# Performance work log

Hardware: AMD Instinct MI355X
Metric: run time of the kernel (lower is better)

The kernel has to match this reference:

```python
import jax, jax.numpy as jnp
import numpy as np

B, L, N = 8, 5, 4096
RADIUS, K = 0.7, 32
SPATIAL_STRIDE = 16
TK, TSTRIDE = 3, 2  # temporal kernel / stride; temporal_padding=[1,1] replicate
DIM, DEPTH, HEADS, DIM_HEAD, MLP_DIM, OUT_DIM = 512, 5, 8, 64, 1024, 1088
INNER = HEADS * DIM_HEAD
N_ANCH = 64
NTOT = N + N_ANCH
M = NTOT // SPATIAL_STRIDE  # spatial anchors per output frame


def setup_inputs() -> dict:
    key = jax.random.key(0)
    ks = list(jax.random.split(key, 16))
    s = 0.02
    p = {}
    p["points"] = jax.random.uniform(ks[0], (B, L, N, 3), jnp.float32, -1.0, 1.0)
    p["conv_d_w"] = jax.random.normal(ks[1], (DIM, 4), jnp.float32) * s
    p["conv_f_w"] = jax.random.normal(ks[2], (DIM, 3), jnp.float32) * s
    p["pos_w"] = jax.random.normal(ks[3], (DIM, 4), jnp.float32) * s
    p["pos_b"] = jnp.zeros((DIM,), jnp.float32)
    p["ln1_g"] = jnp.ones((DEPTH, DIM)); p["ln1_b"] = jnp.zeros((DEPTH, DIM))
    p["qkv_w"] = jax.random.normal(ks[4], (DEPTH, DIM, 3 * INNER), jnp.float32) * s
    p["attn_out_w"] = jax.random.normal(ks[5], (DEPTH, INNER, DIM), jnp.float32) * s
    p["attn_out_b"] = jnp.zeros((DEPTH, DIM))
    p["ln2_g"] = jnp.ones((DEPTH, DIM)); p["ln2_b"] = jnp.zeros((DEPTH, DIM))
    p["ff1_w"] = jax.random.normal(ks[6], (DEPTH, DIM, MLP_DIM), jnp.float32) * s
    p["ff1_b"] = jnp.zeros((DEPTH, MLP_DIM))
    p["ff2_w"] = jax.random.normal(ks[7], (DEPTH, MLP_DIM, DIM), jnp.float32) * s
    p["ff2_b"] = jnp.zeros((DEPTH, DIM))
    p["head_ln_g"] = jnp.ones((DIM,)); p["head_ln_b"] = jnp.zeros((DIM,))
    p["head1_w"] = jax.random.normal(ks[8], (DIM, MLP_DIM), jnp.float32) * s
    p["head1_b"] = jnp.zeros((MLP_DIM,))
    p["head2_w"] = jax.random.normal(ks[9], (MLP_DIM, OUT_DIM), jnp.float32) * s
    p["head2_b"] = jnp.zeros((OUT_DIM,))
    return p


def _layer_norm(x, g, b, eps=1e-5):
    mu = jnp.mean(x, -1, keepdims=True)
    var = jnp.mean((x - mu) ** 2, -1, keepdims=True)
    return (x - mu) * jax.lax.rsqrt(var + eps) * g + b


def _anchor_grid():
    lin = jnp.linspace(-1.5, 1.5, 4)
    gx, gy, gz = jnp.meshgrid(lin, lin, lin, indexing="ij")
    return jnp.stack([gx.ravel(), gy.ravel(), gz.ravel()], -1)  # (64,3)


def _fps(pts, m):
    # furthest point sampling, pts (N,3) -> (m,) int32, first pick is index 0 (pointnet2 semantics)
    def step(carry, _):
        dist, last = carry
        d = jnp.sum((pts - pts[last]) ** 2, -1)
        dist = jnp.minimum(dist, d)
        return (dist, jnp.argmax(dist).astype(jnp.int32)), last
    init = (jnp.full((pts.shape[0],), 1e10, pts.dtype), jnp.int32(0))
    _, idx = jax.lax.scan(step, init, None, length=m)
    return idx


def _ball_query(anchors, pts, radius, k):
    # first k point indices within radius of each anchor; pad with first hit (0 if none)
    d2 = jnp.sum((anchors[:, None, :] - pts[None, :, :]) ** 2, -1)  # (M,N)
    n = pts.shape[0]
    cand = jnp.where(d2 < radius * radius, jnp.arange(n, dtype=jnp.int32), n)
    neg_topk, _ = jax.lax.top_k(-cand, k)  # k smallest indices, ascending
    idx = -neg_topk
    first = idx[:, :1]
    idx = jnp.where(idx == n, first, idx)
    return jnp.where(idx == n, 0, idx)


def _forward(points, conv_d_w, conv_f_w, pos_w, pos_b, ln1_g, ln1_b, qkv_w,
             attn_out_w, attn_out_b, ln2_g, ln2_b, ff1_w, ff1_b, ff2_w, ff2_b,
             head_ln_g, head_ln_b, head1_w, head1_b, head2_w, head2_b):
    anch = _anchor_grid()  # (64,3)
    pts = jnp.concatenate(
        [points[..., :3], jnp.broadcast_to(anch, (B, L, N_ANCH, 3))], axis=2)  # (B,L,NTOT,3)
    # replicate temporal padding [1,1]
    frames = jnp.concatenate([pts[:, :1], pts, pts[:, -1:]], axis=1)  # (B,L+2,NTOT,3)

    trad = (TK - 1) // 2
    nT = L + 2
    gather = jax.vmap(lambda p, i: p[i])
    out_xyz, out_feat = [], []
    for t in range(trad, nT - trad, TSTRIDE):
        f_t = frames[:, t]                                   # (B,NTOT,3)
        a_idx = jax.vmap(lambda p: _fps(p, M))(f_t)          # (B,M)
        a_xyz = gather(f_t, a_idx)                           # (B,M,3)
        feats_w = []
        for i in range(t - trad, t + trad + 1):
            nb = frames[:, i]                                # (B,NTOT,3)
            idx = jax.vmap(lambda a, p: _ball_query(a, p, RADIUS, K))(a_xyz, nb)  # (B,M,K)
            grouped = gather(nb, idx)                        # (B,M,K,3)
            disp = grouped - a_xyz[:, :, None, :]
            tdisp = jnp.full((B, M, K, 1), float(i - t), disp.dtype)
            disp4 = jnp.concatenate([disp, tdisp], -1)       # (B,M,K,4)
            # conv_f(features) + conv_d(displacement); features fed in are the xyz themselves
            feat = (jnp.einsum("bmkc,dc->bmkd", grouped, conv_f_w)
                    + jnp.einsum("bmkc,dc->bmkd", disp4, conv_d_w))
            feats_w.append(jnp.max(feat, axis=2))            # spatial max -> (B,M,DIM)
        out_feat.append(jnp.max(jnp.stack(feats_w, 0), axis=0))  # temporal max
        out_xyz.append(a_xyz)

    nF = len(out_xyz)
    xyzs = jnp.stack(out_xyz, 1)                             # (B,nF,M,3)
    feats = jnp.stack(out_feat, 1).reshape(B, nF * M, DIM)
    tcol = jnp.broadcast_to(
        jnp.arange(1, nF + 1, dtype=xyzs.dtype)[None, :, None, None], (B, nF, M, 1))
    xyzts = jnp.concatenate([xyzs, tcol], -1).reshape(B, nF * M, 4)
    x = jnp.einsum("bnc,dc->bnd", xyzts, pos_w) + pos_b + feats  # (B,T,DIM); emb_relu=False

    scale = DIM_HEAD ** -0.5
    for l in range(DEPTH):
        xn = _layer_norm(x, ln1_g[l], ln1_b[l])
        q, k, v = jnp.split(xn @ qkv_w[l], 3, axis=-1)
        rs = lambda a: a.reshape(B, -1, HEADS, DIM_HEAD)
        q, k, v = rs(q), rs(k), rs(v)
        att = jax.nn.softmax(jnp.einsum("bqhd,bkhd->bhqk", q, k) * scale, axis=-1)
        o = jnp.einsum("bhqk,bkhd->bqhd", att, v).reshape(B, -1, INNER)
        x = x + o @ attn_out_w[l] + attn_out_b[l]
        xn = _layer_norm(x, ln2_g[l], ln2_b[l])
        x = x + jax.nn.gelu(xn @ ff1_w[l] + ff1_b[l], approximate=False) @ ff2_w[l] + ff2_b[l]

    x = jnp.max(x, axis=1)                                   # (B,DIM)
    x = _layer_norm(x, head_ln_g, head_ln_b)
    x = jax.nn.gelu(x @ head1_w + head1_b, approximate=False) @ head2_w + head2_b
    x = x.reshape(B, 1, OUT_DIM // 64, 64)
    x = jax.nn.softmax(x, axis=-1)
    return x @ anch                                          # (B,1,J,3)


def reference(points, conv_d_w, conv_f_w, pos_w, pos_b, ln1_g, ln1_b, qkv_w,
              attn_out_w, attn_out_b, ln2_g, ln2_b, ff1_w, ff1_b, ff2_w, ff2_b,
              head_ln_g, head_ln_b, head1_w, head1_b, head2_w, head2_b):
    return _forward(points, conv_d_w, conv_f_w, pos_w, pos_b, ln1_g, ln1_b, qkv_w,
                    attn_out_w, attn_out_b, ln2_g, ln2_b, ff1_w, ff1_b, ff2_w, ff2_b,
                    head_ln_g, head_ln_b, head1_w, head1_b, head2_w, head2_b)
```

## Files before the change

kernel.cpp:

```cpp
#include <hip/hip_runtime.h>
#include <hip/hip_bf16.h>
#include <cstddef>

#define BB 8
#define LL 5
#define NN 4096
#define NANCH 64
#define NPTS 4160
#define MM 260
#define NFRAME 3
#define SSEQ 780
#define DIMC 512
#define NHEAD 8
#define DHEAD 64
#define MLPD 1024
#define OUTD 1088
#define NROWS 6240
#define VPITCH 784
#define WBUFSZ 2097152

typedef __attribute__((ext_vector_type(8))) short s16x8;
typedef __attribute__((ext_vector_type(4))) float fx4;
typedef unsigned short ushort_t;
typedef unsigned int uint_t;

__device__ __forceinline__ float sqdist_rn(float x1, float y1, float z1,
                                           float x2, float y2, float z2) {
    float dx = __fsub_rn(x1, x2);
    float dy = __fsub_rn(y1, y2);
    float dz = __fsub_rn(z1, z2);
    return __fadd_rn(__fadd_rn(__fmul_rn(dx, dx), __fmul_rn(dy, dy)), __fmul_rn(dz, dz));
}

__device__ __forceinline__ float gelu_exact(float v) {
    return 0.5f * v * (1.0f + erff(v * 0.70710678118654752440f));
}

__device__ __forceinline__ uint_t bf16rn(float f) {
    uint_t u = __float_as_uint(f);
    return (u + 0x7FFFu + ((u >> 16) & 1u)) >> 16;
}
__device__ __forceinline__ void split2(float f, ushort_t& h, ushort_t& l) {
    uint_t hb = bf16rn(f);
    h = (ushort_t)hb;
    float fh = __uint_as_float(hb << 16);
    l = (ushort_t)bf16rn(f - fh);
}

typedef __attribute__((address_space(3))) unsigned int as3u;
typedef const __attribute__((address_space(1))) unsigned int as1u;
__device__ __forceinline__ void gload16(const ushort_t* g, ushort_t* l) {
    __builtin_amdgcn_global_load_lds((as1u*)g, (as3u*)l, 16, 0, 0);
}

template <int CTRL>
__device__ __forceinline__ int dpp_mov(int v) {
    return __builtin_amdgcn_update_dpp(0, v, CTRL, 0xF, 0xF, true);
}
#define DPP_STEP_F(op, v, ctrl) v = op(v, __int_as_float(dpp_mov<ctrl>(__float_as_int(v))))
__device__ __forceinline__ float wave_max_bcast(float v) {
    DPP_STEP_F(fmaxf, v, 0x111); DPP_STEP_F(fmaxf, v, 0x112);
    DPP_STEP_F(fmaxf, v, 0x114); DPP_STEP_F(fmaxf, v, 0x118);
    DPP_STEP_F(fmaxf, v, 0x142); DPP_STEP_F(fmaxf, v, 0x143);
    return __int_as_float(__builtin_amdgcn_readlane(__float_as_int(v), 63));
}
__device__ __forceinline__ float faddf(float a, float b) { return a + b; }
__device__ __forceinline__ float wave_sum_bcast(float v) {
    DPP_STEP_F(faddf, v, 0x111); DPP_STEP_F(faddf, v, 0x112);
    DPP_STEP_F(faddf, v, 0x114); DPP_STEP_F(faddf, v, 0x118);
    DPP_STEP_F(faddf, v, 0x142); DPP_STEP_F(faddf, v, 0x143);
    return __int_as_float(__builtin_amdgcn_readlane(__float_as_int(v), 63));
}

__device__ __forceinline__ void wsplit_tile(
    int bid, int tid, int nthr,
    const float* __restrict__ qkvw, const float* __restrict__ projw,
    const float* __restrict__ ff1w, const float* __restrict__ ff2w,
    ushort_t* __restrict__ th, ushort_t* __restrict__ tl,
    float (*T)[33]) {
    const float* src; int K, N; size_t dst;
    if (bid < 768)       { src = qkvw;  K = 512;  N = 1536; dst = 0;       }
    else if (bid < 1024) { src = projw; K = 512;  N = 512;  dst = 786432;  bid -= 768;  }
    else if (bid < 1536) { src = ff1w;  K = 512;  N = 1024; dst = 1048576; bid -= 1024; }
    else                 { src = ff2w;  K = 1024; N = 512;  dst = 1572864; bid -= 1536; }
    int ntn = N >> 5;
    int tn = bid % ntn, tk = bid / ntn;
    int n0 = tn * 32, k0 = tk * 32;
    for (int e = tid; e < 1024; e += nthr) {
        int r = e >> 5, c = e & 31;
        T[r][c] = src[(size_t)(k0 + r) * N + n0 + c];
    }
    __syncthreads();
    for (int e = tid; e < 1024; e += nthr) {
        int r = e >> 5, c = e & 31;
        ushort_t h, l;
        split2(T[c][r], h, l);
        th[dst + (size_t)(n0 + r) * K + k0 + c] = h;
        tl[dst + (size_t)(n0 + r) * K + k0 + c] = l;
    }
}

__global__ __launch_bounds__(256) void build_pts_kernel(const float* __restrict__ points,
                                                        float* __restrict__ pts) {
    int i = blockIdx.x * 256 + threadIdx.x;
    if (i >= BB * LL * NPTS) return;
    int n = i % NPTS;
    int bl = i / NPTS;
    if (n < NN) {
        const float* src = points + ((size_t)bl * NN + n) * 3;
        pts[(size_t)i * 3 + 0] = src[0];
        pts[(size_t)i * 3 + 1] = src[1];
        pts[(size_t)i * 3 + 2] = src[2];
    } else {
        int j = n - NN;
        int ix = j >> 4, iy = (j >> 2) & 3, iz = j & 3;
        pts[(size_t)i * 3 + 0] = -1.5f + (float)ix;
        pts[(size_t)i * 3 + 1] = -1.5f + (float)iy;
        pts[(size_t)i * 3 + 2] = -1.5f + (float)iz;
    }
}

__global__ __launch_bounds__(256) void fps_ws_kernel(
    const float* __restrict__ pts, float* __restrict__ axyz,
    const float* __restrict__ qkvw, const float* __restrict__ projw,
    const float* __restrict__ ff1w, const float* __restrict__ ff2w,
    ushort_t* __restrict__ th, ushort_t* __restrict__ tl) {
    __shared__ __align__(16) char smem[50048];
    int bid = blockIdx.x;
    int tid = threadIdx.x;
    if (bid >= 24) {
        wsplit_tile(bid - 24, tid, 256, qkvw, projw, ff1w, ff2w, th, tl,
                    (float(*)[33])smem);
        return;
    }
    float* sx = (float*)smem;
    float* sy = sx + NPTS;
    float* sz = sy + NPTS;
    float* redv = sz + NPTS;
    int* redi = (int*)(redv + 8);

    int b = bid / 3, f = bid % 3;
    const float* P = pts + (size_t)(b * LL + 2 * f) * NPTS * 3;
    int lane = tid & 63, wid = tid >> 6;
    int start = tid < 64 ? 17 * tid : 1088 + 16 * (tid - 64);
    float px[17], py[17], pz[17], dist[17];
#pragma unroll
    for (int j = 0; j < 16; j++) {
        int n = start + j;
        float gx = P[(size_t)n * 3 + 0];
        float gy = P[(size_t)n * 3 + 1];
        float gz = P[(size_t)n * 3 + 2];
        px[j] = gx; py[j] = gy; pz[j] = gz;
        sx[n] = gx; sy[n] = gy; sz[n] = gz;
        dist[j] = 1e10f;
    }
    if (tid < 64) {
        int n = start + 16;
        float gx = P[(size_t)n * 3 + 0];
        float gy = P[(size_t)n * 3 + 1];
        float gz = P[(size_t)n * 3 + 2];
        px[16] = gx; py[16] = gy; pz[16] = gz;
        sx[n] = gx; sy[n] = gy; sz[n] = gz;
        dist[16] = 1e10f;
    } else {
        px[16] = 0.f; py[16] = 0.f; pz[16] = 0.f;
        dist[16] = -1.0f;
    }
    __syncthreads();
    float ax = sx[0], ay = sy[0], az = sz[0];
    float* out = axyz + (size_t)bid * MM * 3;
    for (int m = 0; m < MM; m++) {
        if (tid == 0) { out[m * 3 + 0] = ax; out[m * 3 + 1] = ay; out[m * 3 + 2] = az; }
        float bv = -1.0f;
        int bjn = start;
#pragma unroll
        for (int j = 0; j < 16; j++) {
            float d = sqdist_rn(px[j], py[j], pz[j], ax, ay, az);
            float dj = fminf(dist[j], d);
            dist[j] = dj;
            if (dj > bv) { bv = dj; bjn = start + j; }
        }
        if (tid < 64) {
            float d = sqdist_rn(px[16], py[16], pz[16], ax, ay, az);
            float dj = fminf(dist[16], d);
            dist[16] = dj;
            if (dj > bv) { bv = dj; bjn = start + 16; }
        }
        float wmv = wave_max_bcast(bv);
        unsigned long long mk = __ballot(bv == wmv);
        int srcl = __ffsll(mk) - 1;
        int wn = __builtin_amdgcn_readlane(bjn, srcl);
        int par = (m & 1) * 4;
        if (lane == 0) { redv[par + wid] = wmv; redi[par + wid] = wn; }
        __syncthreads();
        float b0 = redv[par + 0], b1 = redv[par + 1];
        float b2 = redv[par + 2], b3 = redv[par + 3];
        int i0 = redi[par + 0], i1 = redi[par + 1];
        int i2 = redi[par + 2], i3 = redi[par + 3];
        float bb = b0; int bn = i0;
        if (b1 > bb) { bb = b1; bn = i1; }
        if (b2 > bb) { bb = b2; bn = i2; }
        if (b3 > bb) { bb = b3; bn = i3; }
        ax = sx[bn]; ay = sy[bn]; az = sz[bn];
    }
}

__global__ __launch_bounds__(64) void group_conv_kernel(
    const float* __restrict__ pts, const float* __restrict__ axyz,
    const float* __restrict__ conv_d_w, const float* __restrict__ conv_f_w,
    const float* __restrict__ pos_w, const float* __restrict__ pos_b,
    float* __restrict__ x) {
    int gid = blockIdx.x;
    int b = gid / SSEQ;
    int rem = gid % SSEQ;
    int f = rem / MM;
    int lane = threadIdx.x;
    const float* A = axyz + (size_t)gid * 3;
    float ax = A[0], ay = A[1], az = A[2];

    float cf0[8], cf1[8], cf2[8], cd0[8], cd1[8], cd2[8], cd3[8], fmx[8];
#pragma unroll
    for (int c = 0; c < 8; c++) {
        int d = lane + 64 * c;
        cf0[c] = conv_f_w[d * 3 + 0];
        cf1[c] = conv_f_w[d * 3 + 1];
        cf2[c] = conv_f_w[d * 3 + 2];
        cd0[c] = conv_d_w[d * 4 + 0];
        cd1[c] = conv_d_w[d * 4 + 1];
        cd2[c] = conv_d_w[d * 4 + 2];
        cd3[c] = conv_d_w[d * 4 + 3];
        fmx[c] = -INFINITY;
    }
    __shared__ int nbr[32];
    __shared__ float gxs[32], gys[32], gzs[32];
    const float R2 = 0.49000000953674316f;

    for (int wi = 0; wi < 3; wi++) {
        int l = 2 * f + wi - 1;
        l = l < 0 ? 0 : (l > 4 ? 4 : l);
        const float* P = pts + (size_t)(b * LL + l) * NPTS * 3;
        int cnt = 0;
        for (int base = 0; base < NPTS && cnt < 32; base += 64) {
            int n = base + lane;
            float d2 = sqdist_rn(P[(size_t)n * 3], P[(size_t)n * 3 + 1], P[(size_t)n * 3 + 2],
                                 ax, ay, az);
            bool hit = d2 < R2;
            unsigned long long mk = __ballot(hit);
            int rank = (int)__popcll(mk & (((unsigned long long)1 << lane) - 1ull));
            if (hit && (cnt + rank) < 32) nbr[cnt + rank] = n;
            cnt += (int)__popcll(mk);
        }
        __syncthreads();
        int eff = cnt < 32 ? cnt : 32;
        if (lane < 32) {
            int idx = (eff == 0) ? 0 : (lane < eff ? nbr[lane] : nbr[0]);
            gxs[lane] = P[(size_t)idx * 3 + 0];
            gys[lane] = P[(size_t)idx * 3 + 1];
            gzs[lane] = P[(size_t)idx * 3 + 2];
        }
        __syncthreads();
        float tf = (float)(wi - 1);
        for (int k = 0; k < 32; k++) {
            float gx = gxs[k], gy = gys[k], gz = gzs[k];
            float dx = gx - ax, dy = gy - ay, dz = gz - az;
#pragma unroll
            for (int c = 0; c < 8; c++) {
                float v = gx * cf0[c] + gy * cf1[c] + gz * cf2[c] +
                          dx * cd0[c] + dy * cd1[c] + dz * cd2[c] + tf * cd3[c];
                fmx[c] = fmaxf(fmx[c], v);
            }
        }
        __syncthreads();
    }
    float tcol = (float)(f + 1);
#pragma unroll
    for (int c = 0; c < 8; c++) {
        int d = lane + 64 * c;
        float pos = ax * pos_w[d * 4 + 0] + ay * pos_w[d * 4 + 1] +
                    az * pos_w[d * 4 + 2] + tcol * pos_w[d * 4 + 3] + pos_b[d];
        x[(size_t)gid * DIMC + d] = fmx[c] + pos;
    }
}

__global__ __launch_bounds__(64) void ln_kernel(const float* __restrict__ x,
                                                const float* __restrict__ g,
                                                const float* __restrict__ b,
                                                ushort_t* __restrict__ yh,
                                                ushort_t* __restrict__ yl) {
    int r = blockIdx.x;
    int lane = threadIdx.x;
    const float* xr = x + (size_t)r * DIMC;
    float4 v0 = *(const float4*)(xr + lane * 8);
    float4 v1 = *(const float4*)(xr + lane * 8 + 4);
    float s = v0.x + v0.y + v0.z + v0.w + v1.x + v1.y + v1.z + v1.w;
    s = wave_sum_bcast(s);
    float mean = s * (1.0f / 512.0f);
    float dv[8];
    dv[0] = v0.x - mean; dv[1] = v0.y - mean; dv[2] = v0.z - mean; dv[3] = v0.w - mean;
    dv[4] = v1.x - mean; dv[5] = v1.y - mean; dv[6] = v1.z - mean; dv[7] = v1.w - mean;
    float sq = 0.f;
#pragma unroll
    for (int c = 0; c < 8; c++) sq += dv[c] * dv[c];
    sq = wave_sum_bcast(sq);
    float var = sq * (1.0f / 512.0f);
    float inv = 1.0f / sqrtf(var + 1e-5f);
    int d = lane * 8;
    ushort_t hs[8], ls[8];
#pragma unroll
    for (int c = 0; c < 8; c++) {
        float v = dv[c] * inv * g[d + c] + b[d + c];
        split2(v, hs[c], ls[c]);
    }
    uint4 hv, lv;
    hv.x = hs[0] | ((uint_t)hs[1] << 16); hv.y = hs[2] | ((uint_t)hs[3] << 16);
    hv.z = hs[4] | ((uint_t)hs[5] << 16); hv.w = hs[6] | ((uint_t)hs[7] << 16);
    lv.x = ls[0] | ((uint_t)ls[1] << 16); lv.y = ls[2] | ((uint_t)ls[3] << 16);
    lv.z = ls[4] | ((uint_t)ls[5] << 16); lv.w = ls[6] | ((uint_t)ls[7] << 16);
    *(uint4*)(yh + (size_t)r * DIMC + d) = hv;
    *(uint4*)(yl + (size_t)r * DIMC + d) = lv;
}

#define BK 32

template <int BN, int EPI>
__global__ __launch_bounds__(256) void gemm_mfma(
    const ushort_t* __restrict__ Ahg, const ushort_t* __restrict__ Alg,
    const ushort_t* __restrict__ Bhg, const ushort_t* __restrict__ Blg,
    const float* __restrict__ bias, const float* __restrict__ R,
    float* __restrict__ C, ushort_t* __restrict__ Ch, ushort_t* __restrict__ Cl,
    ushort_t* __restrict__ Vh, ushort_t* __restrict__ Vl,
    int M, int N, int K) {
    const int WN = BN / 2, NT = WN / 16;
    __shared__ __align__(16) ushort_t Ah[128 * BK];
    __shared__ __align__(16) ushort_t Al[128 * BK];
    __shared__ __align__(16) ushort_t Bh[BN * BK];
    __shared__ __align__(16) ushort_t Bl[BN * BK];
    int tid = threadIdx.x;
    int lane = tid & 63, w = tid >> 6;
    int wm = w & 1, wn = w >> 1;
    int quad = lane >> 4, l15 = lane & 15;

    int nx = gridDim.x;
    int nwg = nx * gridDim.y;
    int lid = blockIdx.x + nx * blockIdx.y;
    int q = nwg >> 3, r = nwg & 7;
    int xcd = lid & 7, off = lid >> 3;
    int nid = (xcd < r ? xcd * (q + 1) : r * (q + 1) + (xcd - r) * q) + off;
    int m0 = (nid / nx) * 128, n0 = (nid % nx) * BN;

    int sr = lane >> 2;
    int sc = lane & 3;
    int kq = ((sc ^ ((sr >> 1) & 3)) << 3);

    int aoff[2];
#pragma unroll
    for (int i = 0; i < 2; i++) {
        int g = w + 4 * i;
        int row = m0 + g * 16 + sr; if (row >= M) row = M - 1;
        aoff[i] = row * K + kq;
    }
    int boff[BN == 128 ? 2 : 1];
    if (BN == 128) {
#pragma unroll
        for (int i = 0; i < 2; i++) {
            int g = w + 4 * i;
            boff[i] = (n0 + g * 16 + sr) * K + kq;
        }
    } else {
        boff[0] = (n0 + w * 16 + sr) * K + kq;
    }

    fx4 acc[4][NT];
#pragma unroll
    for (int mi = 0; mi < 4; mi++)
#pragma unroll
        for (int nj = 0; nj < NT; nj++) acc[mi][nj] = (fx4){0.f, 0.f, 0.f, 0.f};

    int rsw = (l15 >> 1) & 3;
    int aro = (64 * wm + l15) * BK + ((quad ^ rsw) << 3);
    int bro = (WN * wn + l15) * BK + ((quad ^ rsw) << 3);

    for (int k0 = 0; k0 < K; k0 += BK) {
#pragma unroll
        for (int i = 0; i < 2; i++) {
            int g = w + 4 * i;
            gload16(Ahg + aoff[i] + k0, &Ah[g * 16 * BK]);
            gload16(Alg + aoff[i] + k0, &Al[g * 16 * BK]);
        }
        if (BN == 128) {
#pragma unroll
            for (int i = 0; i < 2; i++) {
                int g = w + 4 * i;
                gload16(Bhg + boff[i] + k0, &Bh[g * 16 * BK]);
                gload16(Blg + boff[i] + k0, &Bl[g * 16 * BK]);
            }
        } else {
            gload16(Bhg + boff[0] + k0, &Bh[w * 16 * BK]);
            gload16(Blg + boff[0] + k0, &Bl[w * 16 * BK]);
        }
        __syncthreads();

        s16x8 bf[NT][2];
#pragma unroll
        for (int nj = 0; nj < NT; nj++) {
            bf[nj][0] = *(const s16x8*)&Bh[bro + 16 * nj * BK];
            bf[nj][1] = *(const s16x8*)&Bl[bro + 16 * nj * BK];
        }
#pragma unroll
        for (int mi = 0; mi < 4; mi++) {
            s16x8 aH = *(const s16x8*)&Ah[aro + 16 * mi * BK];
            s16x8 aL = *(const s16x8*)&Al[aro + 16 * mi * BK];
#pragma unroll
            for (int nj = 0; nj < NT; nj++) {
                acc[mi][nj] = __builtin_amdgcn_mfma_f32_16x16x32_bf16(aH, bf[nj][0], acc[mi][nj], 0, 0, 0);
                acc[mi][nj] = __builtin_amdgcn_mfma_f32_16x16x32_bf16(aH, bf[nj][1], acc[mi][nj], 0, 0, 0);
                acc[mi][nj] = __builtin_amdgcn_mfma_f32_16x16x32_bf16(aL, bf[nj][0], acc[mi][nj], 0, 0, 0);
            }
        }
        __syncthreads();
    }
#pragma unroll
    for (int mi = 0; mi < 4; mi++) {
#pragma unroll
        for (int r2 = 0; r2 < 4; r2++) {
            int row = m0 + 64 * wm + 16 * mi + quad * 4 + r2;
            if (row < M) {
#pragma unroll
                for (int nj = 0; nj < NT; nj++) {
                    int col = n0 + WN * wn + 16 * nj + l15;
                    float v = acc[mi][nj][r2];
                    if (EPI == 0) {
                        C[(size_t)row * N + col] = v;
                    } else if (EPI == 3) {
                        C[(size_t)row * N + col] = v + bias[col] + R[(size_t)row * N + col];
                    } else if (EPI == 2) {
                        float gv = gelu_exact(v + bias[col]);
                        ushort_t h, l;
                        split2(gv, h, l);
                        Ch[(size_t)row * N + col] = h;
                        Cl[(size_t)row * N + col] = l;
                    } else if (EPI == 5) {
                        ushort_t h, l;
                        split2(v, h, l);
                        if (col < 1024) {
                            Ch[(size_t)row * 1024 + col] = h;
                            Cl[(size_t)row * 1024 + col] = l;
                        } else {
                            int bb = row / SSEQ, key = row % SSEQ;
                            int hh = (col - 1024) >> 6, dd = (col - 1024) & 63;
                            size_t vo = ((size_t)((bb * 8 + hh) * 64 + dd)) * VPITCH + key;
                            Vh[vo] = h;
                            Vl[vo] = l;
                        }
                    }
                }
            }
        }
    }
}

#define AP 72
#define NATTN 832

__global__ __launch_bounds__(256, 2) void attn_mfma_kernel(
    const ushort_t* __restrict__ qkh, const ushort_t* __restrict__ qkl,
    const ushort_t* __restrict__ vth, const ushort_t* __restrict__ vtl,
    ushort_t* __restrict__ oh, ushort_t* __restrict__ ol,
    const float* __restrict__ nqkvw, const float* __restrict__ nprojw,
    const float* __restrict__ nff1w, const float* __restrict__ nff2w,
    ushort_t* __restrict__ nth, ushort_t* __restrict__ ntl) {
    __shared__ __align__(16) char smem[73728];
    int lid = blockIdx.x;
    if (lid >= NATTN) {
        wsplit_tile(lid - NATTN, threadIdx.x, 256, nqkvw, nprojw, nff1w, nff2w,
                    nth, ntl, (float(*)[33])smem);
        return;
    }
    int xcd = lid & 7, idx = lid >> 3;
    int qt = idx % 13;
    int bh = xcd * 8 + idx / 13;
    int b = bh >> 3, h = bh & 7;

    ushort_t* Qh  = (ushort_t*)smem;
    ushort_t* Ql  = Qh + 64 * AP;
    ushort_t* Kh  = Ql + 64 * AP;
    ushort_t* Kl  = Kh + 64 * AP;
    ushort_t* Vth = Kl + 64 * AP;
    ushort_t* Vtl = Vth + 64 * AP;
    ushort_t* Ph  = Vtl + 64 * AP;
    ushort_t* Pl  = Ph + 64 * AP;

    int tid = threadIdx.x;
    int lane = tid & 63, w = tid >> 6;
    int quad = lane >> 4, l15 = lane & 15;

    int q0 = qt * 64;
    int nq = SSEQ - q0; if (nq > 64) nq = 64;

#pragma unroll
    for (int i = 0; i < 2; i++) {
        int t = tid + 256 * i;
        int row = t >> 3, c = (t & 7) * 8;
        int gq = q0 + (row < nq ? row : nq - 1);
        size_t go = (size_t)(b * SSEQ + gq) * 1024 + h * 64 + c;
        *(uint4*)&Qh[row * AP + c] = *(const uint4*)(qkh + go);
        *(uint4*)&Ql[row * AP + c] = *(const uint4*)(qkl + go);
    }

    fx4 accO[4];
#pragma unroll
    for (int dj = 0; dj < 4; dj++) accO[dj] = (fx4){0.f, 0.f, 0.f, 0.f};
    fx4 accL = (fx4){0.f, 0.f, 0.f, 0.f};

    s16x8 ones;
#pragma unroll
    for (int j = 0; j < 8; j++) ones[j] = (short)16256;

    for (int kt = 0; kt < 13; kt++) {
        int k0 = kt * 64;
        int nk = SSEQ - k0; if (nk > 64) nk = 64;
        __syncthreads();
#pragma unroll
        for (int i = 0; i < 2; i++) {
            int t = tid + 256 * i;
            int row = t >> 3, c = (t & 7) * 8;
            int gk = k0 + (row < nk ? row : nk - 1);
            size_t go = (size_t)(b * SSEQ + gk) * 1024 + h * 64 + c;
            *(uint4*)&Kh[row * AP + c] = *(const uint4*)(qkh + go + 512);
            *(uint4*)&Kl[row * AP + c] = *(const uint4*)(qkl + go + 512);
            size_t vo = ((size_t)(bh * 64 + row)) * VPITCH + k0 + c;
            *(uint4*)&Vth[row * AP + c] = *(const uint4*)(vth + vo);
            *(uint4*)&Vtl[row * AP + c] = *(const uint4*)(vtl + vo);
        }
        __syncthreads();

        fx4 accS[4];
#pragma unroll
        for (int nj = 0; nj < 4; nj++) accS[nj] = (fx4){0.f, 0.f, 0.f, 0.f};
#pragma unroll
        for (int ks = 0; ks < 2; ks++) {
            s16x8 aH = *(const s16x8*)&Qh[(16 * w + l15) * AP + 32 * ks + quad * 8];
            s16x8 aL = *(const s16x8*)&Ql[(16 * w + l15) * AP + 32 * ks + quad * 8];
#pragma unroll
            for (int nj = 0; nj < 4; nj++) {
                s16x8 bH = *(const s16x8*)&Kh[(16 * nj + l15) * AP + 32 * ks + quad * 8];
                s16x8 bL = *(const s16x8*)&Kl[(16 * nj + l15) * AP + 32 * ks + quad * 8];
                accS[nj] = __builtin_amdgcn_mfma_f32_16x16x32_bf16(aH, bH, accS[nj], 0, 0, 0);
                accS[nj] = __builtin_amdgcn_mfma_f32_16x16x32_bf16(aH, bL, accS[nj], 0, 0, 0);
                accS[nj] = __builtin_amdgcn_mfma_f32_16x16x32_bf16(aL, bH, accS[nj], 0, 0, 0);
            }
        }
#pragma unroll
        for (int nj = 0; nj < 4; nj++) {
            int key = 16 * nj + l15;
            bool valid = key < nk;
#pragma unroll
            for (int r = 0; r < 4; r++) {
                float s = accS[nj][r] * 0.125f;
                float p = valid ? __expf(s) : 0.f;
                ushort_t hh, ll;
                split2(p, hh, ll);
                int qrow = 16 * w + quad * 4 + r;
                Ph[qrow * AP + key] = hh;
                Pl[qrow * AP + key] = ll;
            }
        }
#pragma unroll
        for (int ks = 0; ks < 2; ks++) {
            s16x8 aPh = *(const s16x8*)&Ph[(16 * w + l15) * AP + 32 * ks + quad * 8];
            s16x8 aPl = *(const s16x8*)&Pl[(16 * w + l15) * AP + 32 * ks + quad * 8];
            accL = __builtin_amdgcn_mfma_f32_16x16x32_bf16(aPh, ones, accL, 0, 0, 0);
            accL = __builtin_amdgcn_mfma_f32_16x16x32_bf16(aPl, ones, accL, 0, 0, 0);
#pragma unroll
            for (int dj = 0; dj < 4; dj++) {
                s16x8 bVh = *(const s16x8*)&Vth[(16 * dj + l15) * AP + 32 * ks + quad * 8];
                s16x8 bVl = *(const s16x8*)&Vtl[(16 * dj + l15) * AP + 32 * ks + quad * 8];
                accO[dj] = __builtin_amdgcn_mfma_f32_16x16x32_bf16(aPh, bVh, accO[dj], 0, 0, 0);
                accO[dj] = __builtin_amdgcn_mfma_f32_16x16x32_bf16(aPh, bVl, accO[dj], 0, 0, 0);
                accO[dj] = __builtin_amdgcn_mfma_f32_16x16x32_bf16(aPl, bVh, accO[dj], 0, 0, 0);
            }
        }
    }
#pragma unroll
    for (int r = 0; r < 4; r++) {
        int lq = 16 * w + quad * 4 + r;
        if (lq < nq) {
            float inv = 1.0f / accL[r];
            size_t base = (size_t)(b * SSEQ + q0 + lq) * DIMC + h * 64 + l15;
#pragma unroll
            for (int dj = 0; dj < 4; dj++) {
                ushort_t hh, ll;
                split2(accO[dj][r] * inv, hh, ll);
                oh[base + 16 * dj] = hh;
                ol[base + 16 * dj] = ll;
            }
        }
    }
}

__global__ __launch_bounds__(512) void pool_max_kernel(const float* __restrict__ x,
                                                       float* __restrict__ partial) {
    int c = blockIdx.x;
    int bb = blockIdx.y;
    int d = threadIdx.x;
    const float* xb = x + ((size_t)(bb * SSEQ + c * 60)) * DIMC + d;
    float m = -INFINITY;
#pragma unroll 4
    for (int s = 0; s < 60; s++) m = fmaxf(m, xb[(size_t)s * DIMC]);
    partial[((size_t)bb * 13 + c) * DIMC + d] = m;
}

__global__ __launch_bounds__(512) void pool_ln_kernel(const float* __restrict__ partial,
                                                      const float* __restrict__ g,
                                                      const float* __restrict__ b,
                                                      float* __restrict__ out) {
    int bb = blockIdx.x;
    int d = threadIdx.x;
    const float* pb = partial + (size_t)bb * 13 * DIMC + d;
    float m = -INFINITY;
#pragma unroll
    for (int c = 0; c < 13; c++) m = fmaxf(m, pb[(size_t)c * DIMC]);
    __shared__ float col[512];
    __shared__ float red[512];
    col[d] = m;
    red[d] = m;
    __syncthreads();
    for (int s = 256; s > 0; s >>= 1) {
        if (d < s) red[d] += red[d + s];
        __syncthreads();
    }
    float mean = red[0] * (1.0f / 512.0f);
    __syncthreads();
    float dv = col[d] - mean;
    red[d] = dv * dv;
    __syncthreads();
    for (int s = 256; s > 0; s >>= 1) {
        if (d < s) red[d] += red[d + s];
        __syncthreads();
    }
    float var = red[0] * (1.0f / 512.0f);
    float inv = 1.0f / sqrtf(var + 1e-5f);
    out[(size_t)bb * DIMC + d] = dv * inv * g[d] + b[d];
}

__global__ __launch_bounds__(256) void head1_kernel(const float* __restrict__ in,
                                                    const float* __restrict__ W,
                                                    const float* __restrict__ bias,
                                                    float* __restrict__ out) {
    int g = blockIdx.x, bb = blockIdx.y;
    int tid = threadIdx.x;
    int c = tid & 63, ks = tid >> 6;
    int col = g * 64 + c;
    __shared__ float xr[512];
    xr[tid] = in[(size_t)bb * 512 + tid];
    xr[tid + 256] = in[(size_t)bb * 512 + tid + 256];
    __syncthreads();
    float acc = 0.f;
    const float* Wc = W + col;
    for (int k = ks * 128; k < ks * 128 + 128; k++)
        acc += xr[k] * Wc[(size_t)k * MLPD];
    __shared__ float red[256];
    red[tid] = acc;
    __syncthreads();
    if (ks == 0) {
        float v = red[c] + red[c + 64] + red[c + 128] + red[c + 192] + bias[col];
        out[(size_t)bb * MLPD + col] = gelu_exact(v);
    }
}

__global__ __launch_bounds__(256) void head2_kernel(const float* __restrict__ in,
                                                    const float* __restrict__ W,
                                                    const float* __restrict__ bias,
                                                    float* __restrict__ out) {
    int g = blockIdx.x, bb = blockIdx.y;
    int tid = threadIdx.x;
    int c = tid & 63, ks = tid >> 6;
    int col = g * 64 + c;
    __shared__ float xr[1024];
    xr[tid] = in[(size_t)bb * 1024 + tid];
    xr[tid + 256] = in[(size_t)bb * 1024 + tid + 256];
    xr[tid + 512] = in[(size_t)bb * 1024 + tid + 512];
    xr[tid + 768] = in[(size_t)bb * 1024 + tid + 768];
    __syncthreads();
    float acc = 0.f;
    const float* Wc = W + col;
    for (int k = ks * 256; k < ks * 256 + 256; k++)
        acc += xr[k] * Wc[(size_t)k * OUTD];
    __shared__ float red[256];
    red[tid] = acc;
    __syncthreads();
    if (ks == 0) {
        out[(size_t)bb * OUTD + col] = red[c] + red[c + 64] + red[c + 128] + red[c + 192] + bias[col];
    }
}

__global__ __launch_bounds__(64) void smax_anchor_kernel(const float* __restrict__ h2,
                                                         float* __restrict__ out) {
    int bb = blockIdx.x / 17;
    int gcol = blockIdx.x % 17;
    int j = threadIdx.x;
    float v = h2[(size_t)bb * OUTD + gcol * 64 + j];
    float mx = wave_max_bcast(v);
    float p = expf(v - mx);
    float sum = wave_sum_bcast(p);
    int ix = j >> 4, iy = (j >> 2) & 3, iz = j & 3;
    float sx = wave_sum_bcast(p * (-1.5f + (float)ix));
    float sy = wave_sum_bcast(p * (-1.5f + (float)iy));
    float sz = wave_sum_bcast(p * (-1.5f + (float)iz));
    if (j == 0) {
        float* o = out + ((size_t)bb * 17 + gcol) * 3;
        o[0] = sx / sum;
        o[1] = sy / sum;
        o[2] = sz / sum;
    }
}

extern "C" void kernel_launch(void* const* d_in, const int* in_sizes, int n_in,
                              void* d_out, int out_size, void* d_ws, size_t ws_size,
                              hipStream_t stream) {
    const float* points     = (const float*)d_in[0];
    const float* conv_d_w   = (const float*)d_in[1];
    const float* conv_f_w   = (const float*)d_in[2];
    const float* pos_w      = (const float*)d_in[3];
    const float* pos_b      = (const float*)d_in[4];
    const float* ln1_g      = (const float*)d_in[5];
    const float* ln1_b      = (const float*)d_in[6];
    const float* qkv_w      = (const float*)d_in[7];
    const float* attn_out_w = (const float*)d_in[8];
    const float* attn_out_b = (const float*)d_in[9];
    const float* ln2_g      = (const float*)d_in[10];
    const float* ln2_b      = (const float*)d_in[11];
    const float* ff1_w      = (const float*)d_in[12];
    const float* ff1_b      = (const float*)d_in[13];
    const float* ff2_w      = (const float*)d_in[14];
    const float* ff2_b      = (const float*)d_in[15];
    const float* head_ln_g  = (const float*)d_in[16];
    const float* head_ln_b  = (const float*)d_in[17];
    const float* head1_w    = (const float*)d_in[18];
    const float* head1_b    = (const float*)d_in[19];
    const float* head2_w    = (const float*)d_in[20];
    const float* head2_b    = (const float*)d_in[21];

    float* ws = (float*)d_ws;
    float* pts    = ws;
    float* axyz   = pts + 499200;
    float* xbuf   = axyz + 18720;
    float* qkvreg = xbuf + 3194880;
    float* pooled = qkvreg + 9601024;
    float* h1     = pooled + 4096;
    float* h2     = h1 + 8192;
    float* fend   = h2 + 8704;
    ushort_t* qkh = (ushort_t*)qkvreg;
    ushort_t* qkl = qkh + 6389760;
    ushort_t* vth = qkl + 6389760;
    ushort_t* vtl = vth + 3211264;
    ushort_t* us   = (ushort_t*)fend;
    ushort_t* xnh  = us;
    ushort_t* xnl  = xnh + 3194880;
    ushort_t* atth = xnl + 3194880;
    ushort_t* attl = atth + 3194880;
    ushort_t* ffhh = attl + 3194880;
    ushort_t* ffhl = ffhh + 6389760;
    ushort_t* wbh  = ffhl + 6389760;
    ushort_t* wbl  = wbh + 2 * WBUFSZ;
    float* ppart = qkvreg;

    build_pts_kernel<<<650, 256, 0, stream>>>(points, pts);
    fps_ws_kernel<<<24 + 2048, 256, 0, stream>>>(
        pts, axyz, qkv_w, attn_out_w, ff1_w, ff2_w, wbh, wbl);
    group_conv_kernel<<<NROWS, 64, 0, stream>>>(pts, axyz, conv_d_w, conv_f_w,
                                                pos_w, pos_b, xbuf);
    const int MB = (NROWS + 127) / 128;
    for (int l = 0; l < 5; l++) {
        ushort_t* wth = wbh + (size_t)(l & 1) * WBUFSZ;
        ushort_t* wtl = wbl + (size_t)(l & 1) * WBUFSZ;
        ushort_t* nth = wbh + (size_t)((l + 1) & 1) * WBUFSZ;
        ushort_t* ntl = wbl + (size_t)((l + 1) & 1) * WBUFSZ;
        int ln2off = l * 512;
        ln_kernel<<<NROWS, 64, 0, stream>>>(xbuf, ln1_g + ln2off, ln1_b + ln2off, xnh, xnl);
        gemm_mfma<128, 5><<<dim3(1536 / 128, MB), 256, 0, stream>>>(
            xnh, xnl, wth, wtl, nullptr, nullptr, nullptr, qkh, qkl, vth, vtl,
            NROWS, 1536, 512);
        int lnx = l + 1;
        attn_mfma_kernel<<<dim3(l < 4 ? NATTN + 2048 : NATTN), 256, 0, stream>>>(
            qkh, qkl, vth, vtl, atth, attl,
            l < 4 ? qkv_w + (size_t)lnx * 512 * 1536 : nullptr,
            l < 4 ? attn_out_w + (size_t)lnx * 512 * 512 : nullptr,
            l < 4 ? ff1_w + (size_t)lnx * 512 * 1024 : nullptr,
            l < 4 ? ff2_w + (size_t)lnx * 1024 * 512 : nullptr,
            nth, ntl);
        gemm_mfma<64, 3><<<dim3(512 / 64, MB), 256, 0, stream>>>(
            atth, attl, wth + 786432, wtl + 786432, attn_out_b + ln2off, xbuf,
            xbuf, nullptr, nullptr, nullptr, nullptr, NROWS, 512, 512);
        ln_kernel<<<NROWS, 64, 0, stream>>>(xbuf, ln2_g + ln2off, ln2_b + ln2off, xnh, xnl);
        gemm_mfma<128, 2><<<dim3(1024 / 128, MB), 256, 0, stream>>>(
            xnh, xnl, wth + 1048576, wtl + 1048576, ff1_b + l * 1024, nullptr,
            nullptr, ffhh, ffhl, nullptr, nullptr, NROWS, 1024, 512);
        gemm_mfma<64, 3><<<dim3(512 / 64, MB), 256, 0, stream>>>(
            ffhh, ffhl, wth + 1572864, wtl + 1572864, ff2_b + ln2off, xbuf,
            xbuf, nullptr, nullptr, nullptr, nullptr, NROWS, 512, 1024);
    }
    pool_max_kernel<<<dim3(13, BB), 512, 0, stream>>>(xbuf, ppart);
    pool_ln_kernel<<<BB, 512, 0, stream>>>(ppart, head_ln_g, head_ln_b, pooled);
    head1_kernel<<<dim3(16, BB), 256, 0, stream>>>(pooled, head1_w, head1_b, h1);
    head2_kernel<<<dim3(17, BB), 256, 0, stream>>>(h1, head2_w, head2_b, h2);
    smax_anchor_kernel<<<BB * 17, 64, 0, stream>>>(h2, (float*)d_out);
}
```

Measured before the change: 1.810 ms.

## Use direct-to-LDS swizzled loads in attention and register-carried FPS coordinates

The attention kernel now stages Q, K and V tiles with gload16 (likely a global-to-LDS direct load) into unpadded 64-wide rows. It uses an XOR swizzle on column groups in place of padding to avoid bank conflicts, which shrinks shared memory. The FPS kernel no longer copies all points into LDS. It carries the winning point's coordinates through the wave and block reductions, which removes the LDS footprint and the initial barrier. The risks are that the swizzled addressing must match between stores and reads, and that tie-breaking in the reduction must stay consistent with the original index-based selection.

```diff
diff --git a/kernel.cpp b/kernel.cpp
--- a/kernel.cpp
+++ b/kernel.cpp
@@ -125,7 +125,7 @@
     const float* __restrict__ qkvw, const float* __restrict__ projw,
     const float* __restrict__ ff1w, const float* __restrict__ ff2w,
     ushort_t* __restrict__ th, ushort_t* __restrict__ tl) {
-    __shared__ __align__(16) char smem[50048];
+    __shared__ __align__(16) char smem[4352];
     int bid = blockIdx.x;
     int tid = threadIdx.x;
     if (bid >= 24) {
@@ -133,11 +133,10 @@
                     (float(*)[33])smem);
         return;
     }
-    float* sx = (float*)smem;
-    float* sy = sx + NPTS;
-    float* sz = sy + NPTS;
-    float* redv = sz + NPTS;
-    int* redi = (int*)(redv + 8);
+    float* redv = (float*)smem;
+    float* redx = redv + 8;
+    float* redy = redx + 8;
+    float* redz = redy + 8;
 
     int b = bid / 3, f = bid % 3;
     const float* P = pts + (size_t)(b * LL + 2 * f) * NPTS * 3;
@@ -147,61 +146,63 @@
 #pragma unroll
     for (int j = 0; j < 16; j++) {
         int n = start + j;
-        float gx = P[(size_t)n * 3 + 0];
-        float gy = P[(size_t)n * 3 + 1];
-        float gz = P[(size_t)n * 3 + 2];
-        px[j] = gx; py[j] = gy; pz[j] = gz;
-        sx[n] = gx; sy[n] = gy; sz[n] = gz;
+        px[j] = P[(size_t)n * 3 + 0];
+        py[j] = P[(size_t)n * 3 + 1];
+        pz[j] = P[(size_t)n * 3 + 2];
         dist[j] = 1e10f;
     }
     if (tid < 64) {
         int n = start + 16;
-        float gx = P[(size_t)n * 3 + 0];
-        float gy = P[(size_t)n * 3 + 1];
-        float gz = P[(size_t)n * 3 + 2];
-        px[16] = gx; py[16] = gy; pz[16] = gz;
-        sx[n] = gx; sy[n] = gy; sz[n] = gz;
+        px[16] = P[(size_t)n * 3 + 0];
+        py[16] = P[(size_t)n * 3 + 1];
+        pz[16] = P[(size_t)n * 3 + 2];
         dist[16] = 1e10f;
     } else {
         px[16] = 0.f; py[16] = 0.f; pz[16] = 0.f;
         dist[16] = -1.0f;
     }
-    __syncthreads();
-    float ax = sx[0], ay = sy[0], az = sz[0];
+    float ax = P[0], ay = P[1], az = P[2];
     float* out = axyz + (size_t)bid * MM * 3;
     for (int m = 0; m < MM; m++) {
         if (tid == 0) { out[m * 3 + 0] = ax; out[m * 3 + 1] = ay; out[m * 3 + 2] = az; }
         float bv = -1.0f;
-        int bjn = start;
+        float bx = 0.f, by = 0.f, bz = 0.f;
 #pragma unroll
         for (int j = 0; j < 16; j++) {
             float d = sqdist_rn(px[j], py[j], pz[j], ax, ay, az);
             float dj = fminf(dist[j], d);
             dist[j] = dj;
-            if (dj > bv) { bv = dj; bjn = start + j; }
+            if (dj > bv) { bv = dj; bx = px[j]; by = py[j]; bz = pz[j]; }
         }
         if (tid < 64) {
             float d = sqdist_rn(px[16], py[16], pz[16], ax, ay, az);
             float dj = fminf(dist[16], d);
             dist[16] = dj;
-            if (dj > bv) { bv = dj; bjn = start + 16; }
+            if (dj > bv) { bv = dj; bx = px[16]; by = py[16]; bz = pz[16]; }
         }
         float wmv = wave_max_bcast(bv);
         unsigned long long mk = __ballot(bv == wmv);
         int srcl = __ffsll(mk) - 1;
-        int wn = __builtin_amdgcn_readlane(bjn, srcl);
+        float wx = __int_as_float(__builtin_amdgcn_readlane(__float_as_int(bx), srcl));
+        float wy = __int_as_float(__builtin_amdgcn_readlane(__float_as_int(by), srcl));
+        float wz = __int_as_float(__builtin_amdgcn_readlane(__float_as_int(bz), srcl));
         int par = (m & 1) * 4;
-        if (lane == 0) { redv[par + wid] = wmv; redi[par + wid] = wn; }
+        if (lane == 0) {
+            redv[par + wid] = wmv;
+            redx[par + wid] = wx;
+            redy[par + wid] = wy;
+            redz[par + wid] = wz;
+        }
         __syncthreads();
         float b0 = redv[par + 0], b1 = redv[par + 1];
         float b2 = redv[par + 2], b3 = redv[par + 3];
-        int i0 = redi[par + 0], i1 = redi[par + 1];
-        int i2 = redi[par + 2], i3 = redi[par + 3];
-        float bb = b0; int bn = i0;
-        if (b1 > bb) { bb = b1; bn = i1; }
-        if (b2 > bb) { bb = b2; bn = i2; }
-        if (b3 > bb) { bb = b3; bn = i3; }
-        ax = sx[bn]; ay = sy[bn]; az = sz[bn];
+        float x0 = redx[par + 0], x1 = redx[par + 1], x2 = redx[par + 2], x3 = redx[par + 3];
+        float y0 = redy[par + 0], y1 = redy[par + 1], y2 = redy[par + 2], y3 = redy[par + 3];
+        float z0 = redz[par + 0], z1 = redz[par + 1], z2 = redz[par + 2], z3 = redz[par + 3];
+        float bb = b0; ax = x0; ay = y0; az = z0;
+        if (b1 > bb) { bb = b1; ax = x1; ay = y1; az = z1; }
+        if (b2 > bb) { bb = b2; ax = x2; ay = y2; az = z2; }
+        if (b3 > bb) { bb = b3; ax = x3; ay = y3; az = z3; }
     }
 }
 
@@ -459,7 +460,8 @@
     }
 }
 
-#define AP 72
+#define KP2 64
+#define PP 72
 #define NATTN 832
 
 __global__ __launch_bounds__(256, 2) void attn_mfma_kernel(
@@ -469,7 +471,7 @@
     const float* __restrict__ nqkvw, const float* __restrict__ nprojw,
     const float* __restrict__ nff1w, const float* __restrict__ nff2w,
     ushort_t* __restrict__ nth, ushort_t* __restrict__ ntl) {
-    __shared__ __align__(16) char smem[73728];
+    __shared__ __align__(16) char smem[67584];
     int lid = blockIdx.x;
     if (lid >= NATTN) {
         wsplit_tile(lid - NATTN, threadIdx.x, 256, nqkvw, nprojw, nff1w, nff2w,
@@ -482,13 +484,13 @@
     int b = bh >> 3, h = bh & 7;
 
     ushort_t* Qh  = (ushort_t*)smem;
-    ushort_t* Ql  = Qh + 64 * AP;
-    ushort_t* Kh  = Ql + 64 * AP;
-    ushort_t* Kl  = Kh + 64 * AP;
-    ushort_t* Vth = Kl + 64 * AP;
-    ushort_t* Vtl = Vth + 64 * AP;
-    ushort_t* Ph  = Vtl + 64 * AP;
-    ushort_t* Pl  = Ph + 64 * AP;
+    ushort_t* Ql  = Qh + 64 * KP2;
+    ushort_t* Kh  = Ql + 64 * KP2;
+    ushort_t* Kl  = Kh + 64 * KP2;
+    ushort_t* Vth = Kl + 64 * KP2;
+    ushort_t* Vtl = Vth + 64 * KP2;
+    ushort_t* Ph  = Vtl + 64 * KP2;
+    ushort_t* Pl  = Ph + 64 * PP;
 
     int tid = threadIdx.x;
     int lane = tid & 63, w = tid >> 6;
@@ -497,14 +499,17 @@
     int q0 = qt * 64;
     int nq = SSEQ - q0; if (nq > 64) nq = 64;
 
+    int sr8 = lane >> 3;
+    int csw = (lane & 7) ^ sr8;
+
 #pragma unroll
     for (int i = 0; i < 2; i++) {
-        int t = tid + 256 * i;
-        int row = t >> 3, c = (t & 7) * 8;
+        int grp = i * 4 + w;
+        int row = grp * 8 + sr8;
         int gq = q0 + (row < nq ? row : nq - 1);
-        size_t go = (size_t)(b * SSEQ + gq) * 1024 + h * 64 + c;
-        *(uint4*)&Qh[row * AP + c] = *(const uint4*)(qkh + go);
-        *(uint4*)&Ql[row * AP + c] = *(const uint4*)(qkl + go);
+        size_t go = (size_t)(b * SSEQ + gq) * 1024 + h * 64 + csw * 8;
+        gload16(qkh + go, Qh + grp * 512);
+        gload16(qkl + go, Ql + grp * 512);
     }
 
     fx4 accO[4];
@@ -515,6 +520,10 @@
     s16x8 ones;
 #pragma unroll
     for (int j = 0; j < 8; j++) ones[j] = (short)16256;
+
+    int r7 = l15 & 7;
+    int c0 = (quad ^ r7) * 8;
+    int c1 = ((quad ^ r7) ^ 4) * 8;
 
     for (int kt = 0; kt < 13; kt++) {
         int k0 = kt * 64;
@@ -522,15 +531,15 @@
         __syncthreads();
 #pragma unroll
         for (int i = 0; i < 2; i++) {
-            int t = tid + 256 * i;
-            int row = t >> 3, c = (t & 7) * 8;
+            int grp = i * 4 + w;
+            int row = grp * 8 + sr8;
             int gk = k0 + (row < nk ? row : nk - 1);
-            size_t go = (size_t)(b * SSEQ + gk) * 1024 + h * 64 + c;
-            *(uint4*)&Kh[row * AP + c] = *(const uint4*)(qkh + go + 512);
-            *(uint4*)&Kl[row * AP + c] = *(const uint4*)(qkl + go + 512);
-            size_t vo = ((size_t)(bh * 64 + row)) * VPITCH + k0 + c;
-            *(uint4*)&Vth[row * AP + c] = *(const uint4*)(vth + vo);
-            *(uint4*)&Vtl[row * AP + c] = *(const uint4*)(vtl + vo);
+            size_t go = (size_t)(b * SSEQ + gk) * 1024 + h * 64 + 512 + csw * 8;
+            gload16(qkh + go, Kh + grp * 512);
+            gload16(qkl + go, Kl + grp * 512);
+            size_t vo = ((size_t)(bh * 64 + row)) * VPITCH + k0 + csw * 8;
+            gload16(vth + vo, Vth + grp * 512);
+            gload16(vtl + vo, Vtl + grp * 512);
         }
         __syncthreads();
 
@@ -539,12 +548,13 @@
         for (int nj = 0; nj < 4; nj++) accS[nj] = (fx4){0.f, 0.f, 0.f, 0.f};
 #pragma unroll
         for (int ks = 0; ks < 2; ks++) {
-            s16x8 aH = *(const s16x8*)&Qh[(16 * w + l15) * AP + 32 * ks + quad * 8];
-            s16x8 aL = *(const s16x8*)&Ql[(16 * w + l15) * AP + 32 * ks + quad * 8];
+            int ca = ks ? c1 : c0;
+            s16x8 aH = *(const s16x8*)&Qh[(16 * w + l15) * KP2 + ca];
+            s16x8 aL = *(const s16x8*)&Ql[(16 * w + l15) * KP2 + ca];
 #pragma unroll
             for (int nj = 0; nj < 4; nj++) {
-                s16x8 bH = *(const s16x8*)&Kh[(16 * nj + l15) * AP + 32 * ks + quad * 8];
-                s16x8 bL = *(const s16x8*)&Kl[(16 * nj + l15) * AP + 32 * ks + quad * 8];
+                s16x8 bH = *(const s16x8*)&Kh[(16 * nj + l15) * KP2 + ca];
+                s16x8 bL = *(const s16x8*)&Kl[(16 * nj + l15) * KP2 + ca];
                 accS[nj] = __builtin_amdgcn_mfma_f32_16x16x32_bf16(aH, bH, accS[nj], 0, 0, 0);
                 accS[nj] = __builtin_amdgcn_mfma_f32_16x16x32_bf16(aH, bL, accS[nj], 0, 0, 0);
                 accS[nj] = __builtin_amdgcn_mfma_f32_16x16x32_bf16(aL, bH, accS[nj], 0, 0, 0);
@@ -561,20 +571,21 @@
                 ushort_t hh, ll;
                 split2(p, hh, ll);
                 int qrow = 16 * w + quad * 4 + r;
-                Ph[qrow * AP + key] = hh;
-                Pl[qrow * AP + key] = ll;
+                Ph[qrow * PP + key] = hh;
+                Pl[qrow * PP + key] = ll;
             }
         }
 #pragma unroll
         for (int ks = 0; ks < 2; ks++) {
-            s16x8 aPh = *(const s16x8*)&Ph[(16 * w + l15) * AP + 32 * ks + quad * 8];
-            s16x8 aPl = *(const s16x8*)&Pl[(16 * w + l15) * AP + 32 * ks + quad * 8];
+            int ca = ks ? c1 : c0;
+            s16x8 aPh = *(const s16x8*)&Ph[(16 * w + l15) * PP + 32 * ks + quad * 8];
+            s16x8 aPl = *(const s16x8*)&Pl[(16 * w + l15) * PP + 32 * ks + quad * 8];
             accL = __builtin_amdgcn_mfma_f32_16x16x32_bf16(aPh, ones, accL, 0, 0, 0);
             accL = __builtin_amdgcn_mfma_f32_16x16x32_bf16(aPl, ones, accL, 0, 0, 0);
 #pragma unroll
             for (int dj = 0; dj < 4; dj++) {
-                s16x8 bVh = *(const s16x8*)&Vth[(16 * dj + l15) * AP + 32 * ks + quad * 8];
-                s16x8 bVl = *(const s16x8*)&Vtl[(16 * dj + l15) * AP + 32 * ks + quad * 8];
+                s16x8 bVh = *(const s16x8*)&Vth[(16 * dj + l15) * KP2 + ca];
+                s16x8 bVl = *(const s16x8*)&Vtl[(16 * dj + l15) * KP2 + ca];
                 accO[dj] = __builtin_amdgcn_mfma_f32_16x16x32_bf16(aPh, bVh, accO[dj], 0, 0, 0);
                 accO[dj] = __builtin_amdgcn_mfma_f32_16x16x32_bf16(aPh, bVl, accO[dj], 0, 0, 0);
                 accO[dj] = __builtin_amdgcn_mfma_f32_16x16x32_bf16(aPl, bVh, accO[dj], 0, 0, 0);
```

Measured after the change: 1.777 ms. About the same (-1.8%).
